# Performance work log

Measured on AMD Instinct MI355X. Metric: run time of the kernel, lower is better.

Reference implementation:

```python
import jax, jax.numpy as jnp
import numpy as np

DECAY = 0.99
EPSILON = 1e-05
NUM_CODES = 4096
CODE_DIM = 64
B, S = 16, 4096


def setup_inputs() -> dict:
    key = jax.random.key(0)
    k1, k2, k3 = jax.random.split(key, 3)
    x = jax.random.normal(k1, (B, S, CODE_DIM), dtype=jnp.float32)
    codebook = jax.random.normal(k2, (NUM_CODES, CODE_DIM), dtype=jnp.float32)
    cluster_size = jnp.zeros((NUM_CODES,), dtype=jnp.float32)
    ema_w = jax.random.normal(k3, (NUM_CODES, CODE_DIM), dtype=jnp.float32)
    return {"x": x, "codebook": codebook, "cluster_size": cluster_size, "ema_w": ema_w}


def reference(x, codebook, cluster_size, ema_w):
    Bd, Sd, D = x.shape
    flat_x = x.reshape(-1, D)  # [N, D], N = B*S
    # Monotone in true cdist(p=2), so argmin is identical to torch.cdist(...).argmin.
    x_sq = jnp.sum(flat_x * flat_x, axis=-1, keepdims=True)          # [N, 1]
    c_sq = jnp.sum(codebook * codebook, axis=-1)                     # [K]
    d2 = x_sq - 2.0 * (flat_x @ codebook.T) + c_sq[None, :]          # [N, K]
    indices = jnp.argmin(d2, axis=-1)                                # [N] int
    quantized = jnp.take(codebook, indices, axis=0).reshape(Bd, Sd, D)
    # Training-path EMA update (one-hot scatter-accumulate, done via segment ops).
    batch_cluster = jax.ops.segment_sum(
        jnp.ones_like(indices, dtype=flat_x.dtype), indices, num_segments=NUM_CODES)
    embed_sum = jax.ops.segment_sum(flat_x, indices, num_segments=NUM_CODES)  # [K, D]
    new_cluster_size = DECAY * cluster_size + (1.0 - DECAY) * batch_cluster
    new_ema_w = DECAY * ema_w + (1.0 - DECAY) * embed_sum
    n = jnp.sum(new_cluster_size)
    smoothed = (new_cluster_size + EPSILON) / (n + NUM_CODES * EPSILON) * n
    new_codebook = new_ema_w / smoothed[:, None]
    return (quantized, indices.reshape(Bd, Sd), new_codebook, new_cluster_size, new_ema_w)
```

## Files before the change

kernel.cpp:

```cpp
#include <hip/hip_runtime.h>

#define NUM_CODES 4096
#define CODE_DIM  64
#define NPTS      65536
#define NTILES    (NUM_CODES / 16)
#define NSEG2     8
#define SEGTILES  (NTILES / NSEG2)
#define NCOPY     8
#define DECAYF    0.99f
#define EPSF      1e-5f
#define BIASF     512.0f
#define THRF      0.0625f

typedef __attribute__((ext_vector_type(8))) short short8v;
typedef __attribute__((ext_vector_type(4))) float f32x4;
#define MFMA16 __builtin_amdgcn_mfma_f32_16x16x32_bf16

__device__ __forceinline__ unsigned med3u(unsigned a, unsigned b, unsigned c) {
    unsigned d;
    asm("v_med3_u32 %0, %1, %2, %3" : "=v"(d) : "v"(a), "v"(b), "v"(c));
    return d;
}
__device__ __forceinline__ unsigned min3u(unsigned a, unsigned b, unsigned c) {
    unsigned d;
    asm("v_min3_u32 %0, %1, %2, %3" : "=v"(d) : "v"(a), "v"(b), "v"(c));
    return d;
}
__device__ __forceinline__ unsigned minu(unsigned a, unsigned b) { return a < b ? a : b; }
__device__ __forceinline__ unsigned maxu(unsigned a, unsigned b) { return a > b ? a : b; }

#define WS_BC   0
#define WS_ES   32768
#define WS_N    2129920
#define WS_CNT  2129921
#define WS_CSQ  2129924
#define WS_CF   2134020
#define WS_TOP2 2396164

#define OUT_Q    0
#define OUT_IDX  4194304
#define OUT_CB   4259840
#define OUT_CS   4521984
#define OUT_EMA  4526080

__device__ __forceinline__ unsigned short f2bf(float f) {
    unsigned u = __float_as_uint(f);
    u += 0x7FFFu + ((u >> 16) & 1u);
    return (unsigned short)(u >> 16);
}
__device__ __forceinline__ float bf2f(unsigned short h) {
    return __uint_as_float(((unsigned)h) << 16);
}

__global__ __launch_bounds__(256) void prep_all(const float* __restrict__ cb,
                                                const float* __restrict__ cs_in,
                                                float* __restrict__ csq,
                                                short* __restrict__ cf,
                                                float* __restrict__ n_out) {
    if (blockIdx.x == 128) {
        __shared__ float ws4[4];
        int tid = threadIdx.x;
        float s = 0.f;
#pragma unroll
        for (int j = 0; j < 16; ++j) s += cs_in[tid + 256 * j];
#pragma unroll
        for (int off = 32; off > 0; off >>= 1) s += __shfl_down(s, off);
        if ((tid & 63) == 0) ws4[tid >> 6] = s;
        __syncthreads();
        if (tid == 0)
            n_out[0] = DECAYF * (ws4[0] + ws4[1] + ws4[2] + ws4[3])
                     + (1.0f - DECAYF) * (float)NPTS;
        return;
    }
    int t     = blockIdx.x * 256 + threadIdx.x;
    int code  = t >> 3;
    int chunk = t & 7;
    int khalf = chunk >> 2;
    int g     = chunk & 3;
    const float* src = cb + (size_t)code * CODE_DIM + khalf * 32 + g * 8;
    float4 v0 = *(const float4*)(src);
    float4 v1 = *(const float4*)(src + 4);
    float f[8] = {v0.x, v0.y, v0.z, v0.w, v1.x, v1.y, v1.z, v1.w};
    float sq = 0.f;
    short8v H, L;
#pragma unroll
    for (int j = 0; j < 8; ++j) {
        sq = fmaf(f[j], f[j], sq);
        float s = -2.0f * f[j];
        unsigned short hb = f2bf(s);
        H[j] = (short)hb;
        L[j] = (short)f2bf(s - bf2f(hb));
    }
#pragma unroll
    for (int off = 1; off < 8; off <<= 1) sq += __shfl_xor(sq, off);
    if (chunk == 0) csq[code] = sq + BIASF;
    int ctile = code >> 4;
    int lane_in_frag = g * 16 + (code & 15);
    *(short8v*)(cf + ((size_t)(ctile * 4 + khalf) * 64 + lane_in_frag) * 8)     = H;
    *(short8v*)(cf + ((size_t)(ctile * 4 + 2 + khalf) * 64 + lane_in_frag) * 8) = L;
}

__global__ __launch_bounds__(256) void scan_mfma(const float* __restrict__ x,
                                                 const short* __restrict__ cf,
                                                 const float* __restrict__ csq,
                                                 uint2* __restrict__ top2) {
    const int wid  = threadIdx.x >> 6;
    const int lane = threadIdx.x & 63;
    const int blk  = blockIdx.x;
    const int pw   = blk >> 1;
    const int seg  = (blk & 1) * 4 + wid;
    const int col  = lane & 15;
    const int grp  = lane >> 4;
    const unsigned grpsh = (unsigned)(grp << 2);
    const int pbase = pw * 64;

    short8v xh[4][2], xl[4][2];
#pragma unroll
    for (int t = 0; t < 4; ++t) {
#pragma unroll
        for (int h = 0; h < 2; ++h) {
            const float* xp = x + (size_t)(pbase + t * 16 + col) * CODE_DIM + h * 32 + grp * 8;
            float4 v0 = *(const float4*)(xp);
            float4 v1 = *(const float4*)(xp + 4);
            float f[8] = {v0.x, v0.y, v0.z, v0.w, v1.x, v1.y, v1.z, v1.w};
            short8v H, L;
#pragma unroll
            for (int j = 0; j < 8; ++j) {
                unsigned short hb = f2bf(f[j]);
                H[j] = (short)hb;
                L[j] = (short)f2bf(f[j] - bf2f(hb));
            }
            xh[t][h] = H; xl[t][h] = L;
        }
    }

    unsigned m1k[4], m2k[4];
#pragma unroll
    for (int t = 0; t < 4; ++t) { m1k[t] = 0xFFFFFFFFu; m2k[t] = 0xFFFFFFFFu; }

#define LOAD_TILE(CT, AF, CQ) do { \
    const short* p_ = cf + ((size_t)(CT) * 4 * 64 + lane) * 8; \
    AF[0] = *(const short8v*)(p_); \
    AF[1] = *(const short8v*)(p_ + 64 * 8); \
    AF[2] = *(const short8v*)(p_ + 2 * 64 * 8); \
    AF[3] = *(const short8v*)(p_ + 3 * 64 * 8); \
    CQ = *(const f32x4*)(csq + (CT) * 16 + grp * 4); } while(0)

#define COMPUTE_TILE(CT, AF, CQ) do { \
    const unsigned tb9_ = (unsigned)(((CT) - tb) << 4) | grpsh; \
    unsigned idx_[4] = {tb9_, tb9_ | 1u, tb9_ | 2u, tb9_ | 3u}; \
    _Pragma("unroll") \
    for (int t = 0; t < 4; ++t) { \
        f32x4 a = CQ; \
        a = MFMA16(AF[0], xh[t][0], a, 0, 0, 0); \
        a = MFMA16(AF[1], xh[t][1], a, 0, 0, 0); \
        a = MFMA16(AF[0], xl[t][0], a, 0, 0, 0); \
        a = MFMA16(AF[1], xl[t][1], a, 0, 0, 0); \
        a = MFMA16(AF[2], xh[t][0], a, 0, 0, 0); \
        a = MFMA16(AF[3], xh[t][1], a, 0, 0, 0); \
        _Pragma("unroll") \
        for (int r = 0; r < 4; ++r) { \
            unsigned key = (__float_as_uint(a[r]) & 0xFFFFFE00u) | idx_[r]; \
            m2k[t] = med3u(m1k[t], m2k[t], key); \
            m1k[t] = minu(m1k[t], key); \
        } \
    } } while(0)

    short8v A0[4], A1[4];
    f32x4 q0, q1;
    const int tb = seg * SEGTILES;
    LOAD_TILE(tb, A0, q0);
#pragma unroll 4
    for (int it = 0; it < SEGTILES / 2; ++it) {
        const int t0 = tb + 2 * it, t1 = t0 + 1;
        const int t2 = (2 * it + 2 < SEGTILES) ? t1 + 1 : tb;
        LOAD_TILE(t1, A1, q1);
        COMPUTE_TILE(t0, A0, q0);
        LOAD_TILE(t2, A0, q0);
        COMPUTE_TILE(t1, A1, q1);
    }
#undef LOAD_TILE
#undef COMPUTE_TILE

#pragma unroll
    for (int t = 0; t < 4; ++t) {
#pragma unroll
        for (int off = 16; off <= 32; off <<= 1) {
            unsigned o1 = __shfl_xor(m1k[t], off);
            unsigned o2 = __shfl_xor(m2k[t], off);
            m2k[t] = min3u(maxu(m1k[t], o1), m2k[t], o2);
            m1k[t] = minu(m1k[t], o1);
        }
    }
    if (lane < 16) {
#pragma unroll
        for (int t = 0; t < 4; ++t)
            top2[(size_t)seg * NPTS + pbase + t * 16 + lane] = make_uint2(m1k[t], m2k[t]);
    }
}

__global__ __launch_bounds__(256) void emit1(const uint2* __restrict__ top2,
                                             float* __restrict__ idx_out,
                                             float* __restrict__ bc_acc,
                                             int* __restrict__ flagged,
                                             int* __restrict__ cnt) {
    const int p = blockIdx.x * 256 + threadIdx.x;
    const int lane = threadIdx.x & 63;
    unsigned M1 = 0xFFFFFFFFu, M2 = 0xFFFFFFFFu;
    int wseg = 0;
#pragma unroll
    for (int s = 0; s < NSEG2; ++s) {
        uint2 t = top2[(size_t)s * NPTS + p];
        M2 = min3u(maxu(M1, t.x), M2, t.y);
        if (t.x < M1) wseg = s;
        M1 = minu(M1, t.x);
    }
    float m1v = __uint_as_float(M1 & 0xFFFFFE00u);
    float m2v = __uint_as_float(M2 & 0xFFFFFE00u);
    unsigned bits = M1 & 0x1FFu;
    int code = (wseg * SEGTILES + (int)(bits >> 4)) * 16 + (int)((bits >> 2) & 3u) * 4 + (int)(bits & 3u);

    bool certified = (m2v - m1v >= THRF);
    if (certified) {
        idx_out[p] = (float)code;
        atomicAdd(&bc_acc[(blockIdx.x & (NCOPY - 1)) * NUM_CODES + code], 1.0f);
    }
    unsigned long long mask = __ballot(!certified);
    int nw = __popcll(mask);
    int base = 0;
    if (lane == 0 && nw) base = atomicAdd(cnt, nw);
    base = __shfl(base, 0);
    if (!certified) {
        int off = __popcll(mask & ((1ULL << lane) - 1ULL));
        flagged[base + off] = p;
    }
}

__global__ __launch_bounds__(64) void fallback_kernel(const float* __restrict__ x,
                                                      const float* __restrict__ cb,
                                                      const int* __restrict__ flagged,
                                                      const int* __restrict__ cnt,
                                                      float* __restrict__ idx_out,
                                                      float* __restrict__ bc_acc) {
    __shared__ float xs[CODE_DIM];
    const int lane = threadIdx.x;
    const int n = *cnt;
    float* bcc = bc_acc + (size_t)(blockIdx.x & (NCOPY - 1)) * NUM_CODES;
    for (int w = blockIdx.x; w < n; w += 1024) {
        const int p = flagged[w];
        xs[lane] = x[(size_t)p * CODE_DIM + lane];
        __syncthreads();
        float4 xv[16];
#pragma unroll
        for (int q = 0; q < 16; ++q) xv[q] = *(const float4*)(xs + q * 4);
        double best = 1e300; int bi = 0;
        for (int j = 0; j < 64; ++j) {
            const int c = lane + 64 * j;
            const float4* cp = (const float4*)(cb + (size_t)c * CODE_DIM);
            double a0 = 0.0, a1 = 0.0, a2 = 0.0, a3 = 0.0;
#pragma unroll
            for (int q = 0; q < 16; ++q) {
                float4 cv = cp[q];
                double d0 = (double)xv[q].x - (double)cv.x;
                double d1 = (double)xv[q].y - (double)cv.y;
                double d2 = (double)xv[q].z - (double)cv.z;
                double d3 = (double)xv[q].w - (double)cv.w;
                a0 = fma(d0, d0, a0);
                a1 = fma(d1, d1, a1);
                a2 = fma(d2, d2, a2);
                a3 = fma(d3, d3, a3);
            }
            double acc = (a0 + a1) + (a2 + a3);
            if (acc < best) { best = acc; bi = c; }
        }
#pragma unroll
        for (int off = 1; off < 64; off <<= 1) {
            double ob = __shfl_xor(best, off);
            int   obi = __shfl_xor(bi, off);
            if (ob < best || (ob == best && obi < bi)) { best = ob; bi = obi; }
        }
        if (lane == 0) {
            idx_out[p] = (float)bi;
            atomicAdd(&bcc[bi], 1.0f);
        }
        __syncthreads();
    }
}

__global__ __launch_bounds__(256) void emit2(const float* __restrict__ x,
                                             const float* __restrict__ cb,
                                             const float* __restrict__ idx_out,
                                             float* __restrict__ q_out,
                                             float* __restrict__ es_acc) {
    const int p    = blockIdx.x * 4 + (threadIdx.x >> 6);
    const int lane = threadIdx.x & 63;
    const int fin  = (int)idx_out[p];
    float* esc = es_acc + (size_t)(blockIdx.x & (NCOPY - 1)) * (NUM_CODES * CODE_DIM);
    float xv = x[(size_t)p * CODE_DIM + lane];
    float cv = cb[(size_t)fin * CODE_DIM + lane];
    q_out[(size_t)p * CODE_DIM + lane] = cv;
    atomicAdd(&esc[(size_t)fin * CODE_DIM + lane], xv);
}

__global__ __launch_bounds__(256) void finalize_kernel(const float* __restrict__ cs_in,
                                                       const float* __restrict__ ema_in,
                                                       const float* __restrict__ bc_acc,
                                                       const float* __restrict__ es_acc,
                                                       const float* __restrict__ n_ptr,
                                                       float* __restrict__ cs_out,
                                                       float* __restrict__ ema_out,
                                                       float* __restrict__ cb_out) {
    int idx = blockIdx.x * 256 + threadIdx.x;
    int k   = idx >> 6;
    float bc = 0.f, es = 0.f;
#pragma unroll
    for (int c = 0; c < NCOPY; ++c) {
        bc += bc_acc[(size_t)c * NUM_CODES + k];
        es += es_acc[(size_t)c * (NUM_CODES * CODE_DIM) + idx];
    }
    float ncs = DECAYF * cs_in[k] + (1.0f - DECAYF) * bc;
    if ((idx & 63) == 0) cs_out[k] = ncs;
    float n = *n_ptr;
    float smoothed = (ncs + EPSF) / (n + (float)NUM_CODES * EPSF) * n;
    float ew = DECAYF * ema_in[idx] + (1.0f - DECAYF) * es;
    ema_out[idx] = ew;
    cb_out[idx]  = ew / smoothed;
}

extern "C" void kernel_launch(void* const* d_in, const int* in_sizes, int n_in,
                              void* d_out, int out_size, void* d_ws, size_t ws_size,
                              hipStream_t stream) {
    const float* x    = (const float*)d_in[0];
    const float* cb   = (const float*)d_in[1];
    const float* cs   = (const float*)d_in[2];
    const float* emaw = (const float*)d_in[3];
    float* out = (float*)d_out;
    float* ws  = (float*)d_ws;

    hipMemsetAsync(ws, 0, (size_t)(WS_CNT + 1) * sizeof(float), stream);

    prep_all<<<129, 256, 0, stream>>>(cb, cs, ws + WS_CSQ, (short*)(ws + WS_CF), ws + WS_N);

    scan_mfma<<<(NPTS / 64) * NSEG2 / 4, 256, 0, stream>>>(
        x, (const short*)(ws + WS_CF), ws + WS_CSQ, (uint2*)(ws + WS_TOP2));

    emit1<<<NPTS / 256, 256, 0, stream>>>(
        (const uint2*)(ws + WS_TOP2), out + OUT_IDX, ws + WS_BC,
        (int*)(ws + WS_CF), (int*)(ws + WS_CNT));

    fallback_kernel<<<1024, 64, 0, stream>>>(
        x, cb, (const int*)(ws + WS_CF), (const int*)(ws + WS_CNT),
        out + OUT_IDX, ws + WS_BC);

    emit2<<<NPTS / 4, 256, 0, stream>>>(
        x, cb, out + OUT_IDX, out + OUT_Q, ws + WS_ES);

    finalize_kernel<<<(NUM_CODES * CODE_DIM) / 256, 256, 0, stream>>>(
        cs, emaw, ws + WS_BC, ws + WS_ES, ws + WS_N,
        out + OUT_CS, out + OUT_EMA, out + OUT_CB);
}
```

Measured before the change: 310.4 us.

## Narrow scan segments, tighten certification bias, and use fp32 top-2 fallback with fp64 refine

Splits the codebook scan into 16 segments instead of 8, which frees one key bit so the distance keys keep more mantissa precision. The bias and certification threshold are lowered so fewer points get flagged. The fallback now computes distances in fp32 with one point per wave and four waves per block, and keeps the top-2 candidates. Those two are then rechecked in fp64 to pick the final index. This removes slow fp64 work from the full 4096-code scan, at the cost of twice as much top2 traffic in emit1 and a small risk if the true nearest code falls outside the fp32 top-2.

New measurement: 327.4 us. +5.5%, slower.

```diff
diff --git a/kernel.cpp b/kernel.cpp
--- a/kernel.cpp
+++ b/kernel.cpp
@@ -4,13 +4,13 @@
 #define CODE_DIM  64
 #define NPTS      65536
 #define NTILES    (NUM_CODES / 16)
-#define NSEG2     8
+#define NSEG2     16
 #define SEGTILES  (NTILES / NSEG2)
 #define NCOPY     8
 #define DECAYF    0.99f
 #define EPSF      1e-5f
-#define BIASF     512.0f
-#define THRF      0.0625f
+#define BIASF     160.0f
+#define THRF      0.02f
 
 typedef __attribute__((ext_vector_type(8))) short short8v;
 typedef __attribute__((ext_vector_type(4))) float f32x4;
@@ -28,6 +28,12 @@
 }
 __device__ __forceinline__ unsigned minu(unsigned a, unsigned b) { return a < b ? a : b; }
 __device__ __forceinline__ unsigned maxu(unsigned a, unsigned b) { return a > b ? a : b; }
+
+#define UPDL(v, c, M1, I1, M2, I2) do{ \
+    bool lt1_ = (v) < (M1) || ((v) == (M1) && (c) < (I1)); \
+    bool lt2_ = (v) < (M2) || ((v) == (M2) && (c) < (I2)); \
+    if (lt1_) { M2 = M1; I2 = I1; M1 = (v); I1 = (c); } \
+    else if (lt2_) { M2 = (v); I2 = (c); } } while(0)
 
 #define WS_BC   0
 #define WS_ES   32768
@@ -107,8 +113,8 @@
     const int wid  = threadIdx.x >> 6;
     const int lane = threadIdx.x & 63;
     const int blk  = blockIdx.x;
-    const int pw   = blk >> 1;
-    const int seg  = (blk & 1) * 4 + wid;
+    const int pw   = blk >> 2;
+    const int seg  = (blk & 3) * 4 + wid;
     const int col  = lane & 15;
     const int grp  = lane >> 4;
     const unsigned grpsh = (unsigned)(grp << 2);
@@ -147,8 +153,8 @@
     CQ = *(const f32x4*)(csq + (CT) * 16 + grp * 4); } while(0)
 
 #define COMPUTE_TILE(CT, AF, CQ) do { \
-    const unsigned tb9_ = (unsigned)(((CT) - tb) << 4) | grpsh; \
-    unsigned idx_[4] = {tb9_, tb9_ | 1u, tb9_ | 2u, tb9_ | 3u}; \
+    const unsigned tb8_ = (unsigned)(((CT) - tb) << 4) | grpsh; \
+    unsigned idx_[4] = {tb8_, tb8_ | 1u, tb8_ | 2u, tb8_ | 3u}; \
     _Pragma("unroll") \
     for (int t = 0; t < 4; ++t) { \
         f32x4 a = CQ; \
@@ -160,7 +166,7 @@
         a = MFMA16(AF[3], xh[t][1], a, 0, 0, 0); \
         _Pragma("unroll") \
         for (int r = 0; r < 4; ++r) { \
-            unsigned key = (__float_as_uint(a[r]) & 0xFFFFFE00u) | idx_[r]; \
+            unsigned key = (__float_as_uint(a[r]) & 0xFFFFFF00u) | idx_[r]; \
             m2k[t] = med3u(m1k[t], m2k[t], key); \
             m1k[t] = minu(m1k[t], key); \
         } \
@@ -215,9 +221,9 @@
         if (t.x < M1) wseg = s;
         M1 = minu(M1, t.x);
     }
-    float m1v = __uint_as_float(M1 & 0xFFFFFE00u);
-    float m2v = __uint_as_float(M2 & 0xFFFFFE00u);
-    unsigned bits = M1 & 0x1FFu;
+    float m1v = __uint_as_float(M1 & 0xFFFFFF00u);
+    float m2v = __uint_as_float(M2 & 0xFFFFFF00u);
+    unsigned bits = M1 & 0xFFu;
     int code = (wseg * SEGTILES + (int)(bits >> 4)) * 16 + (int)((bits >> 2) & 3u) * 4 + (int)(bits & 3u);
 
     bool certified = (m2v - m1v >= THRF);
@@ -236,54 +242,70 @@
     }
 }
 
-__global__ __launch_bounds__(64) void fallback_kernel(const float* __restrict__ x,
-                                                      const float* __restrict__ cb,
-                                                      const int* __restrict__ flagged,
-                                                      const int* __restrict__ cnt,
-                                                      float* __restrict__ idx_out,
-                                                      float* __restrict__ bc_acc) {
-    __shared__ float xs[CODE_DIM];
-    const int lane = threadIdx.x;
+__global__ __launch_bounds__(256) void fallback_kernel(const float* __restrict__ x,
+                                                       const float* __restrict__ cb,
+                                                       const int* __restrict__ flagged,
+                                                       const int* __restrict__ cnt,
+                                                       float* __restrict__ idx_out,
+                                                       float* __restrict__ bc_acc) {
+    const int wid  = threadIdx.x >> 6;
+    const int lane = threadIdx.x & 63;
     const int n = *cnt;
     float* bcc = bc_acc + (size_t)(blockIdx.x & (NCOPY - 1)) * NUM_CODES;
-    for (int w = blockIdx.x; w < n; w += 1024) {
+    for (int w = blockIdx.x * 4 + wid; w < n; w += 2048) {
         const int p = flagged[w];
-        xs[lane] = x[(size_t)p * CODE_DIM + lane];
-        __syncthreads();
+        const float4* xp = (const float4*)(x + (size_t)p * CODE_DIM);
         float4 xv[16];
 #pragma unroll
-        for (int q = 0; q < 16; ++q) xv[q] = *(const float4*)(xs + q * 4);
-        double best = 1e300; int bi = 0;
+        for (int q = 0; q < 16; ++q) xv[q] = xp[q];
+
+        float m1 = 3e38f, m2 = 3e38f;
+        int   i1 = 0,     i2 = 0;
         for (int j = 0; j < 64; ++j) {
             const int c = lane + 64 * j;
             const float4* cp = (const float4*)(cb + (size_t)c * CODE_DIM);
-            double a0 = 0.0, a1 = 0.0, a2 = 0.0, a3 = 0.0;
+            float a0 = 0.f, a1 = 0.f, a2 = 0.f, a3 = 0.f;
 #pragma unroll
             for (int q = 0; q < 16; ++q) {
                 float4 cv = cp[q];
-                double d0 = (double)xv[q].x - (double)cv.x;
-                double d1 = (double)xv[q].y - (double)cv.y;
-                double d2 = (double)xv[q].z - (double)cv.z;
-                double d3 = (double)xv[q].w - (double)cv.w;
-                a0 = fma(d0, d0, a0);
-                a1 = fma(d1, d1, a1);
-                a2 = fma(d2, d2, a2);
-                a3 = fma(d3, d3, a3);
+                float d0 = xv[q].x - cv.x;
+                float d1 = xv[q].y - cv.y;
+                float d2 = xv[q].z - cv.z;
+                float d3 = xv[q].w - cv.w;
+                a0 = fmaf(d0, d0, a0);
+                a1 = fmaf(d1, d1, a1);
+                a2 = fmaf(d2, d2, a2);
+                a3 = fmaf(d3, d3, a3);
             }
-            double acc = (a0 + a1) + (a2 + a3);
-            if (acc < best) { best = acc; bi = c; }
+            float acc = (a0 + a1) + (a2 + a3);
+            if (acc < m1)      { m2 = m1; i2 = i1; m1 = acc; i1 = c; }
+            else if (acc < m2) { m2 = acc; i2 = c; }
         }
 #pragma unroll
         for (int off = 1; off < 64; off <<= 1) {
-            double ob = __shfl_xor(best, off);
-            int   obi = __shfl_xor(bi, off);
-            if (ob < best || (ob == best && obi < bi)) { best = ob; bi = obi; }
+            float om1 = __shfl_xor(m1, off); int oi1 = __shfl_xor(i1, off);
+            float om2 = __shfl_xor(m2, off); int oi2 = __shfl_xor(i2, off);
+            UPDL(om1, oi1, m1, i1, m2, i2);
+            UPDL(om2, oi2, m1, i1, m2, i2);
+        }
+        double xd  = (double)x[(size_t)p * CODE_DIM + lane];
+        double c1d = (double)cb[(size_t)i1 * CODE_DIM + lane];
+        double c2d = (double)cb[(size_t)i2 * CODE_DIM + lane];
+        double d1 = xd - c1d, d2 = xd - c2d;
+        double e1 = d1 * d1, e2 = d2 * d2;
+#pragma unroll
+        for (int off = 1; off < 64; off <<= 1) {
+            e1 += __shfl_xor(e1, off);
+            e2 += __shfl_xor(e2, off);
         }
         if (lane == 0) {
-            idx_out[p] = (float)bi;
-            atomicAdd(&bcc[bi], 1.0f);
-        }
-        __syncthreads();
+            int fin;
+            if (e1 < e2)      fin = i1;
+            else if (e2 < e1) fin = i2;
+            else              fin = (i1 < i2) ? i1 : i2;
+            idx_out[p] = (float)fin;
+            atomicAdd(&bcc[fin], 1.0f);
+        }
     }
 }
 
@@ -348,7 +370,7 @@
         (const uint2*)(ws + WS_TOP2), out + OUT_IDX, ws + WS_BC,
         (int*)(ws + WS_CF), (int*)(ws + WS_CNT));
 
-    fallback_kernel<<<1024, 64, 0, stream>>>(
+    fallback_kernel<<<512, 256, 0, stream>>>(
         x, cb, (const int*)(ws + WS_CF), (const int*)(ws + WS_CNT),
         out + OUT_IDX, ws + WS_BC);
 
```
